# Optimization experiments

Hardware: AMD Instinct MI355X
Metric: run time of the kernel (lower is better)

The kernel has to match this reference:

```python
import jax, jax.numpy as jnp
import numpy as np

B, S, D = 2, 2048, 1024
H = 16
HD = D // H

def setup_inputs() -> dict:
    key = jax.random.key(0)
    k1, k2, k3 = jax.random.split(key, 3)
    x = jax.random.normal(k1, (B, S, D), dtype=jnp.float32)
    w_attn = jax.random.normal(k2, (D, 3 * D), dtype=jnp.float32) * (1.0 / np.sqrt(D))
    b_attn = jnp.zeros((3 * D,), dtype=jnp.float32)
    w_proj = jax.random.normal(k3, (D, D), dtype=jnp.float32) * (1.0 / np.sqrt(D))
    b_proj = jnp.zeros((D,), dtype=jnp.float32)
    return {"x": x, "w_attn": w_attn, "b_attn": b_attn, "w_proj": w_proj, "b_proj": b_proj}

def reference(x, w_attn, b_attn, w_proj, b_proj):
    bsz, seq_len, embed_dim = x.shape
    qkv = x @ w_attn + b_attn                      # [B,S,3D]
    q, k, v = jnp.split(qkv, 3, axis=-1)
    # [B,S,D] -> [B,H,S,HD]
    def heads(t):
        return t.reshape(bsz, seq_len, H, HD).transpose(0, 2, 1, 3)
    q, k, v = heads(q), heads(k), heads(v)
    scale = 1.0 / np.sqrt(HD)
    att = jnp.einsum('bhqd,bhkd->bhqk', q, k) * scale  # [B,H,S,S]
    causal = jnp.tril(jnp.ones((seq_len, seq_len), dtype=bool))
    att = jnp.where(causal[None, None], att, jnp.float32(-jnp.inf))
    att = jax.nn.softmax(att, axis=-1)
    y = jnp.einsum('bhqk,bhkd->bhqd', att, v)          # [B,H,S,HD]
    y = y.transpose(0, 2, 1, 3).reshape(bsz, seq_len, embed_dim)
    return y @ w_proj + b_proj
```

## Files before the change

kernel.cpp:

```cpp
#include <hip/hip_runtime.h>
#include <hip/hip_bf16.h>
#include <math.h>

typedef __bf16 bf16x8 __attribute__((ext_vector_type(8)));
typedef float f32x4 __attribute__((ext_vector_type(4)));

#define LOG2E 1.44269504088896340736f

#define SEQ 2048
#define DMODEL 1024
#define NH 16
#define HD 64

__device__ __forceinline__ void gl2lds16(const void* g, void* l) {
  __builtin_amdgcn_global_load_lds((__attribute__((address_space(1))) void*)g,
                                   (__attribute__((address_space(3))) void*)l,
                                   16, 0, 0);
}

__global__ void detect_dtype(const unsigned* __restrict__ x, unsigned* __restrict__ flag) {
  __shared__ int cnt[256];
  int c = 0;
  for (int i = threadIdx.x; i < 4096; i += 256) {
    unsigned e = (x[i] >> 23) & 0xFF;
    c += (e >= 0x70 && e <= 0x8F) ? 1 : 0;
  }
  cnt[threadIdx.x] = c;
  __syncthreads();
  for (int s = 128; s > 0; s >>= 1) {
    if ((int)threadIdx.x < s) cnt[threadIdx.x] += cnt[threadIdx.x + s];
    __syncthreads();
  }
  if (threadIdx.x == 0) flag[0] = (cnt[0] > 2048) ? 1u : 0u;
}

__global__ void conv_to_bf16(const void* __restrict__ in, __hip_bfloat16* __restrict__ out,
                             int n, const unsigned* __restrict__ flag) {
  const int i = (blockIdx.x * 256 + threadIdx.x) * 4;
  if (i >= n) return;
  if (*flag) {
    const float4 v = *(const float4*)((const float*)in + i);
    out[i + 0] = __float2bfloat16(v.x);
    out[i + 1] = __float2bfloat16(v.y);
    out[i + 2] = __float2bfloat16(v.z);
    out[i + 3] = __float2bfloat16(v.w);
  } else {
    const __hip_bfloat16* bin = (const __hip_bfloat16*)in;
    out[i + 0] = bin[i + 0];
    out[i + 1] = bin[i + 1];
    out[i + 2] = bin[i + 2];
    out[i + 3] = bin[i + 3];
  }
}

__global__ void transpose_cvt(const void* __restrict__ in, __hip_bfloat16* __restrict__ out,
                              int R, int C, const unsigned* __restrict__ flag) {
  __shared__ __hip_bfloat16 tile[64][65];
  const bool f32 = (*flag != 0);
  const int c0 = blockIdx.x * 64, r0 = blockIdx.y * 64;
  const int tx = threadIdx.x & 63, ty = threadIdx.x >> 6;
#pragma unroll
  for (int i = 0; i < 16; ++i) {
    int r = ty + i * 4;
    long idx = (long)(r0 + r) * C + c0 + tx;
    tile[r][tx] = f32 ? __float2bfloat16(((const float*)in)[idx])
                      : ((const __hip_bfloat16*)in)[idx];
  }
  __syncthreads();
#pragma unroll
  for (int i = 0; i < 16; ++i) {
    int r = ty + i * 4;
    out[(long)(c0 + r) * R + r0 + tx] = tile[tx][r];
  }
}

template <int MODE>
__global__ __launch_bounds__(256, 2) void gemm_bt(
    const __hip_bfloat16* __restrict__ A, const __hip_bfloat16* __restrict__ Bt,
    const __hip_bfloat16* __restrict__ bias, void* __restrict__ C,
    __hip_bfloat16* __restrict__ q_ws, __hip_bfloat16* __restrict__ k_ws,
    __hip_bfloat16* __restrict__ vt_ws, int M, int N, int K,
    const unsigned* __restrict__ flag) {
  alignas(16) __shared__ __hip_bfloat16 lA[128 * 32];
  alignas(16) __shared__ __hip_bfloat16 lB[128 * 32];
  const int tid = threadIdx.x;
  const int wave = tid >> 6, lane = tid & 63;
  const int l15 = lane & 15, lq = lane >> 4;
  const int m0 = blockIdx.y * 128, n0 = blockIdx.x * 128;
  const int wrow = (wave >> 1) * 64, wcol = (wave & 1) * 64;

  const __hip_bfloat16* ap0 = A + (long)(m0 + wave * 16 + (lane >> 2)) * K + (lane & 3) * 8;
  const __hip_bfloat16* bp0 = Bt + (long)(n0 + wave * 16 + (lane >> 2)) * K + (lane & 3) * 8;
  __hip_bfloat16* lA0 = lA + wave * 512;
  __hip_bfloat16* lA1 = lA + (wave + 4) * 512;
  __hip_bfloat16* lB0 = lB + wave * 512;
  __hip_bfloat16* lB1 = lB + (wave + 4) * 512;

  f32x4 acc[4][4];
#pragma unroll
  for (int i = 0; i < 4; ++i)
#pragma unroll
    for (int j = 0; j < 4; ++j) acc[i][j] = {0.f, 0.f, 0.f, 0.f};

  for (int k0 = 0; k0 < K; k0 += 32) {
    __syncthreads();
    gl2lds16(ap0 + k0, lA0);
    gl2lds16(ap0 + (long)64 * K + k0, lA1);
    gl2lds16(bp0 + k0, lB0);
    gl2lds16(bp0 + (long)64 * K + k0, lB1);
    __syncthreads();
    bf16x8 af[4], bfr[4];
#pragma unroll
    for (int i = 0; i < 4; ++i)
      af[i] = *(const bf16x8*)(lA + (wrow + 16 * i + l15) * 32 + lq * 8);
#pragma unroll
    for (int j = 0; j < 4; ++j)
      bfr[j] = *(const bf16x8*)(lB + (wcol + 16 * j + l15) * 32 + lq * 8);
#pragma unroll
    for (int i = 0; i < 4; ++i)
#pragma unroll
      for (int j = 0; j < 4; ++j)
        acc[i][j] = __builtin_amdgcn_mfma_f32_16x16x32_bf16(af[i], bfr[j], acc[i][j], 0, 0, 0);
  }

  const bool outf32 = (MODE == 0) && (*flag != 0);
#pragma unroll
  for (int i = 0; i < 4; ++i) {
    const int row = m0 + wrow + 16 * i + lq * 4;
#pragma unroll
    for (int j = 0; j < 4; ++j) {
      const int col = n0 + wcol + 16 * j + l15;
      const float bv = __bfloat162float(bias[col]);
#pragma unroll
      for (int r = 0; r < 4; ++r) {
        const float v = acc[i][j][r] + bv;
        const int rr = row + r;
        if (MODE == 0) {
          if (outf32)
            ((float*)C)[(long)rr * N + col] = v;
          else
            ((__hip_bfloat16*)C)[(long)rr * N + col] = __float2bfloat16(v);
        } else {
          const int which = col >> 10;
          const int f = col & 1023;
          const int h = f >> 6, d = f & 63;
          const int b = rr >> 11, s = rr & 2047;
          const long bh = (long)b * NH + h;
          const __hip_bfloat16 hv = __float2bfloat16(v);
          if (which == 0)
            q_ws[(bh * SEQ + s) * HD + d] = hv;
          else if (which == 1)
            k_ws[(bh * SEQ + s) * HD + d] = hv;
          else
            vt_ws[(bh * HD + d) * SEQ + s] = hv;
        }
      }
    }
  }
}

__global__ __launch_bounds__(256, 4) void attn_fused(
    const __hip_bfloat16* __restrict__ q_ws, const __hip_bfloat16* __restrict__ k_ws,
    const __hip_bfloat16* __restrict__ vt_ws, __hip_bfloat16* __restrict__ y_ws) {
  alignas(16) __shared__ __hip_bfloat16 lK[2][64 * 64];
  alignas(16) __shared__ __hip_bfloat16 lV[2][64 * 64];
  alignas(16) __shared__ __hip_bfloat16 lP[4][16 * 72];
  const int tid = threadIdx.x, wave = tid >> 6, lane = tid & 63;
  const int l15 = lane & 15, lq = lane >> 4;
  const int bh = blockIdx.x >> 4, pair = blockIdx.x & 15;
  const __hip_bfloat16* Qb = q_ws + (long)bh * SEQ * HD;
  const __hip_bfloat16* Kb = k_ws + (long)bh * SEQ * HD;
  const __hip_bfloat16* Vb = vt_ws + (long)bh * HD * SEQ;
  __hip_bfloat16* lPw = lP[wave];
  const int b = bh >> 4, h = bh & 15;
  const float SCL = 0.125f * LOG2E;

  const int p0 = wave * 16 + (lane >> 3);
  const int cl = lane & 7;

#pragma unroll 1
  for (int phase = 0; phase < 2; ++phase) {
    const int qt = phase ? (31 - pair) : pair;
    const int q0 = qt * 64;
    const int nkt = qt + 1;

    const int qrow = q0 + wave * 16 + l15;
    const bf16x8 qa0 = *(const bf16x8*)(Qb + (long)qrow * HD + lq * 8);
    const bf16x8 qa1 = *(const bf16x8*)(Qb + (long)qrow * HD + 32 + lq * 8);

    f32x4 accO[4];
#pragma unroll
    for (int j = 0; j < 4; ++j) accO[j] = {0.f, 0.f, 0.f, 0.f};
    float l_part[4];
#pragma unroll
    for (int r = 0; r < 4; ++r) l_part[r] = 0.f;

#pragma unroll
    for (int i = 0; i < 2; ++i) {
      const int p = p0 + i * 8;
      const int c = cl ^ (p & 7);
      gl2lds16(Kb + (long)p * HD + c * 8, &lK[0][(wave * 16 + i * 8) * 64]);
      gl2lds16(Vb + (long)p * SEQ + c * 8, &lV[0][(wave * 16 + i * 8) * 64]);
    }
    __syncthreads();

#pragma unroll 1
    for (int kt = 0; kt < nkt; ++kt) {
      const int buf = kt & 1;
      if (kt + 1 < nkt) {
        const int kb = (kt + 1) * 64;
#pragma unroll
        for (int i = 0; i < 2; ++i) {
          const int p = p0 + i * 8;
          const int c = cl ^ (p & 7);
          gl2lds16(Kb + (long)(kb + p) * HD + c * 8, &lK[buf ^ 1][(wave * 16 + i * 8) * 64]);
          gl2lds16(Vb + (long)p * SEQ + kb + c * 8, &lV[buf ^ 1][(wave * 16 + i * 8) * 64]);
        }
      }
      const __hip_bfloat16* lKb = lK[buf];
      const __hip_bfloat16* lVb = lV[buf];

      f32x4 sf[4];
#pragma unroll
      for (int jt = 0; jt < 4; ++jt) {
        sf[jt] = {0.f, 0.f, 0.f, 0.f};
        const int pp = jt * 16 + l15;
        const bf16x8 kb0 = *(const bf16x8*)(lKb + (pp * 8 + (lq ^ (pp & 7))) * 8);
        const bf16x8 kb1 = *(const bf16x8*)(lKb + (pp * 8 + ((4 + lq) ^ (pp & 7))) * 8);
        sf[jt] = __builtin_amdgcn_mfma_f32_16x16x32_bf16(qa0, kb0, sf[jt], 0, 0, 0);
        sf[jt] = __builtin_amdgcn_mfma_f32_16x16x32_bf16(qa1, kb1, sf[jt], 0, 0, 0);
      }

      const bool diag = (kt == nkt - 1);
#pragma unroll
      for (int r = 0; r < 4; ++r) {
        float p[4];
#pragma unroll
        for (int jt = 0; jt < 4; ++jt) p[jt] = exp2f(sf[jt][r] * SCL);
        if (diag) {
          const int rloc = wave * 16 + lq * 4 + r;
#pragma unroll
          for (int jt = 0; jt < 4; ++jt) {
            const int col = jt * 16 + l15;
            p[jt] = (col <= rloc) ? p[jt] : 0.f;
          }
        }
        l_part[r] += (p[0] + p[1]) + (p[2] + p[3]);
#pragma unroll
        for (int jt = 0; jt < 4; ++jt)
          lPw[(lq * 4 + r) * 72 + jt * 16 + l15] = __float2bfloat16(p[jt]);
      }

      const bf16x8 pa0 = *(const bf16x8*)(lPw + l15 * 72 + lq * 8);
      const bf16x8 pa1 = *(const bf16x8*)(lPw + l15 * 72 + 32 + lq * 8);
#pragma unroll
      for (int j = 0; j < 4; ++j) {
        const int d = j * 16 + l15;
        const bf16x8 vb0 = *(const bf16x8*)(lVb + (d * 8 + (lq ^ (d & 7))) * 8);
        const bf16x8 vb1 = *(const bf16x8*)(lVb + (d * 8 + ((4 + lq) ^ (d & 7))) * 8);
        accO[j] = __builtin_amdgcn_mfma_f32_16x16x32_bf16(pa0, vb0, accO[j], 0, 0, 0);
        accO[j] = __builtin_amdgcn_mfma_f32_16x16x32_bf16(pa1, vb1, accO[j], 0, 0, 0);
      }
      __syncthreads();
    }

#pragma unroll
    for (int r = 0; r < 4; ++r) {
      float l = l_part[r];
#pragma unroll
      for (int off = 1; off < 16; off <<= 1) l += __shfl_xor(l, off, 64);
      const float inv = 1.f / l;
      const int s = q0 + wave * 16 + lq * 4 + r;
#pragma unroll
      for (int j = 0; j < 4; ++j) {
        const float v = accO[j][r] * inv;
        y_ws[((long)(b * SEQ + s)) * DMODEL + h * HD + j * 16 + l15] = __float2bfloat16(v);
      }
    }
  }
}

extern "C" void kernel_launch(void* const* d_in, const int* in_sizes, int n_in,
                              void* d_out, int out_size, void* d_ws, size_t ws_size,
                              hipStream_t stream) {
  const void* x = d_in[0];
  const void* w_attn = d_in[1];
  const void* b_attn = d_in[2];
  const void* w_proj = d_in[3];
  const void* b_proj = d_in[4];

  char* ws = (char*)d_ws;
  const size_t MB = 1024 * 1024;
  unsigned* flag = (unsigned*)ws;
  __hip_bfloat16* wT_attn = (__hip_bfloat16*)(ws + 1 * MB);
  __hip_bfloat16* wT_proj = (__hip_bfloat16*)(ws + 7 * MB);
  __hip_bfloat16* x_bf = (__hip_bfloat16*)(ws + 9 * MB);
  __hip_bfloat16* q_ws = (__hip_bfloat16*)(ws + 17 * MB);
  __hip_bfloat16* k_ws = (__hip_bfloat16*)(ws + 25 * MB);
  __hip_bfloat16* vt_ws = (__hip_bfloat16*)(ws + 33 * MB);
  __hip_bfloat16* y_ws = (__hip_bfloat16*)(ws + 41 * MB);
  __hip_bfloat16* bA_bf = (__hip_bfloat16*)(ws + 49 * MB);
  __hip_bfloat16* bP_bf = (__hip_bfloat16*)(ws + 49 * MB + 8192);

  detect_dtype<<<1, 256, 0, stream>>>((const unsigned*)x, flag);

  conv_to_bf16<<<4096, 256, 0, stream>>>(x, x_bf, 4194304, flag);
  conv_to_bf16<<<3, 256, 0, stream>>>(b_attn, bA_bf, 3072, flag);
  conv_to_bf16<<<1, 256, 0, stream>>>(b_proj, bP_bf, 1024, flag);
  transpose_cvt<<<dim3(3072 / 64, 1024 / 64), 256, 0, stream>>>(w_attn, wT_attn, 1024, 3072, flag);
  transpose_cvt<<<dim3(1024 / 64, 1024 / 64), 256, 0, stream>>>(w_proj, wT_proj, 1024, 1024, flag);

  gemm_bt<1><<<dim3(3072 / 128, 4096 / 128), 256, 0, stream>>>(
      x_bf, wT_attn, bA_bf, nullptr, q_ws, k_ws, vt_ws, 4096, 3072, 1024, flag);

  attn_fused<<<dim3(512), 256, 0, stream>>>(q_ws, k_ws, vt_ws, y_ws);

  gemm_bt<0><<<dim3(1024 / 128, 4096 / 128), 256, 0, stream>>>(
      y_ws, wT_proj, bP_bf, d_out, nullptr, nullptr, nullptr, 4096, 1024, 1024, flag);
}
```

Measured before the change: 227.6 us.

## Compute transposed scores to keep P in registers and permute V layout

The attention kernel now computes S^T (K as the A operand, Q as B), so each lane's softmax outputs line up with the B-operand layout of the PV MFMA. That removes the per-wave LDS round trip for P. The QKV GEMM writes V^T with a permuted sequence order within each 32-element group, so the register-resident P columns match the V fragments. The grid also changes from 512 blocks that each process a paired short and long query tile to 1024 blocks that each handle one tile, with heavy tiles scheduled first. Output stores become 4-wide vectors and the row-sum reduction needs fewer shuffles.

```diff
diff --git a/kernel.cpp b/kernel.cpp
--- a/kernel.cpp
+++ b/kernel.cpp
@@ -3,6 +3,7 @@
 #include <math.h>
 
 typedef __bf16 bf16x8 __attribute__((ext_vector_type(8)));
+typedef __bf16 bf16x4 __attribute__((ext_vector_type(4)));
 typedef float f32x4 __attribute__((ext_vector_type(4)));
 
 #define LOG2E 1.44269504088896340736f
@@ -151,8 +152,14 @@
             q_ws[(bh * SEQ + s) * HD + d] = hv;
           else if (which == 1)
             k_ws[(bh * SEQ + s) * HD + d] = hv;
-          else
-            vt_ws[(bh * HD + d) * SEQ + s] = hv;
+          else {
+            const int w = s & 31;
+            const int wl = w & 15;
+            const int sig = (w >> 4) ? (2 * (wl & ~3) + 4 + (wl & 3))
+                                     : (2 * (wl & ~3) + (wl & 3));
+            const int sp = (s & ~31) | sig;
+            vt_ws[(bh * HD + d) * SEQ + sp] = hv;
+          }
         }
       }
     }
@@ -164,119 +171,110 @@
     const __hip_bfloat16* __restrict__ vt_ws, __hip_bfloat16* __restrict__ y_ws) {
   alignas(16) __shared__ __hip_bfloat16 lK[2][64 * 64];
   alignas(16) __shared__ __hip_bfloat16 lV[2][64 * 64];
-  alignas(16) __shared__ __hip_bfloat16 lP[4][16 * 72];
   const int tid = threadIdx.x, wave = tid >> 6, lane = tid & 63;
   const int l15 = lane & 15, lq = lane >> 4;
-  const int bh = blockIdx.x >> 4, pair = blockIdx.x & 15;
+  const int qt = 31 - (blockIdx.x >> 5);
+  const int bh = blockIdx.x & 31;
+  const int q0 = qt * 64;
+  const int nkt = qt + 1;
   const __hip_bfloat16* Qb = q_ws + (long)bh * SEQ * HD;
   const __hip_bfloat16* Kb = k_ws + (long)bh * SEQ * HD;
   const __hip_bfloat16* Vb = vt_ws + (long)bh * HD * SEQ;
-  __hip_bfloat16* lPw = lP[wave];
   const int b = bh >> 4, h = bh & 15;
   const float SCL = 0.125f * LOG2E;
 
+  const int qrow = q0 + wave * 16 + l15;
+  const bf16x8 qa0 = *(const bf16x8*)(Qb + (long)qrow * HD + lq * 8);
+  const bf16x8 qa1 = *(const bf16x8*)(Qb + (long)qrow * HD + 32 + lq * 8);
+
+  f32x4 accO[4];
+#pragma unroll
+  for (int j = 0; j < 4; ++j) accO[j] = {0.f, 0.f, 0.f, 0.f};
+  float l_part = 0.f;
+
   const int p0 = wave * 16 + (lane >> 3);
   const int cl = lane & 7;
 
+#pragma unroll
+  for (int i = 0; i < 2; ++i) {
+    const int p = p0 + i * 8;
+    const int c = cl ^ (p & 7);
+    gl2lds16(Kb + (long)p * HD + c * 8, &lK[0][(wave * 16 + i * 8) * 64]);
+    gl2lds16(Vb + (long)p * SEQ + c * 8, &lV[0][(wave * 16 + i * 8) * 64]);
+  }
+  __syncthreads();
+
 #pragma unroll 1
-  for (int phase = 0; phase < 2; ++phase) {
-    const int qt = phase ? (31 - pair) : pair;
-    const int q0 = qt * 64;
-    const int nkt = qt + 1;
-
-    const int qrow = q0 + wave * 16 + l15;
-    const bf16x8 qa0 = *(const bf16x8*)(Qb + (long)qrow * HD + lq * 8);
-    const bf16x8 qa1 = *(const bf16x8*)(Qb + (long)qrow * HD + 32 + lq * 8);
-
-    f32x4 accO[4];
-#pragma unroll
-    for (int j = 0; j < 4; ++j) accO[j] = {0.f, 0.f, 0.f, 0.f};
-    float l_part[4];
-#pragma unroll
-    for (int r = 0; r < 4; ++r) l_part[r] = 0.f;
-
-#pragma unroll
-    for (int i = 0; i < 2; ++i) {
-      const int p = p0 + i * 8;
-      const int c = cl ^ (p & 7);
-      gl2lds16(Kb + (long)p * HD + c * 8, &lK[0][(wave * 16 + i * 8) * 64]);
-      gl2lds16(Vb + (long)p * SEQ + c * 8, &lV[0][(wave * 16 + i * 8) * 64]);
-    }
-    __syncthreads();
-
-#pragma unroll 1
-    for (int kt = 0; kt < nkt; ++kt) {
-      const int buf = kt & 1;
-      if (kt + 1 < nkt) {
-        const int kb = (kt + 1) * 64;
-#pragma unroll
-        for (int i = 0; i < 2; ++i) {
-          const int p = p0 + i * 8;
-          const int c = cl ^ (p & 7);
-          gl2lds16(Kb + (long)(kb + p) * HD + c * 8, &lK[buf ^ 1][(wave * 16 + i * 8) * 64]);
-          gl2lds16(Vb + (long)p * SEQ + kb + c * 8, &lV[buf ^ 1][(wave * 16 + i * 8) * 64]);
+  for (int kt = 0; kt < nkt; ++kt) {
+    const int buf = kt & 1;
+    if (kt + 1 < nkt) {
+      const int kb = (kt + 1) * 64;
+#pragma unroll
+      for (int i = 0; i < 2; ++i) {
+        const int p = p0 + i * 8;
+        const int c = cl ^ (p & 7);
+        gl2lds16(Kb + (long)(kb + p) * HD + c * 8, &lK[buf ^ 1][(wave * 16 + i * 8) * 64]);
+        gl2lds16(Vb + (long)p * SEQ + kb + c * 8, &lV[buf ^ 1][(wave * 16 + i * 8) * 64]);
+      }
+    }
+    const __hip_bfloat16* lKb = lK[buf];
+    const __hip_bfloat16* lVb = lV[buf];
+
+    f32x4 st[4];
+#pragma unroll
+    for (int t = 0; t < 4; ++t) {
+      st[t] = {0.f, 0.f, 0.f, 0.f};
+      const int pp = t * 16 + l15;
+      const bf16x8 kb0 = *(const bf16x8*)(lKb + (pp * 8 + (lq ^ (pp & 7))) * 8);
+      const bf16x8 kb1 = *(const bf16x8*)(lKb + (pp * 8 + ((4 + lq) ^ (pp & 7))) * 8);
+      st[t] = __builtin_amdgcn_mfma_f32_16x16x32_bf16(kb0, qa0, st[t], 0, 0, 0);
+      st[t] = __builtin_amdgcn_mfma_f32_16x16x32_bf16(kb1, qa1, st[t], 0, 0, 0);
+    }
+
+    const bool diag = (kt == nkt - 1);
+    const int qloc = wave * 16 + l15;
+    bf16x8 pb[2];
+#pragma unroll
+    for (int c = 0; c < 2; ++c) {
+#pragma unroll
+      for (int t2 = 0; t2 < 2; ++t2) {
+        const int tt = c * 2 + t2;
+#pragma unroll
+        for (int r = 0; r < 4; ++r) {
+          float pv = exp2f(st[tt][r] * SCL);
+          if (diag) {
+            const int colloc = tt * 16 + lq * 4 + r;
+            pv = (colloc <= qloc) ? pv : 0.f;
+          }
+          l_part += pv;
+          pb[c][t2 * 4 + r] = (__bf16)pv;
         }
       }
-      const __hip_bfloat16* lKb = lK[buf];
-      const __hip_bfloat16* lVb = lV[buf];
-
-      f32x4 sf[4];
-#pragma unroll
-      for (int jt = 0; jt < 4; ++jt) {
-        sf[jt] = {0.f, 0.f, 0.f, 0.f};
-        const int pp = jt * 16 + l15;
-        const bf16x8 kb0 = *(const bf16x8*)(lKb + (pp * 8 + (lq ^ (pp & 7))) * 8);
-        const bf16x8 kb1 = *(const bf16x8*)(lKb + (pp * 8 + ((4 + lq) ^ (pp & 7))) * 8);
-        sf[jt] = __builtin_amdgcn_mfma_f32_16x16x32_bf16(qa0, kb0, sf[jt], 0, 0, 0);
-        sf[jt] = __builtin_amdgcn_mfma_f32_16x16x32_bf16(qa1, kb1, sf[jt], 0, 0, 0);
-      }
-
-      const bool diag = (kt == nkt - 1);
-#pragma unroll
-      for (int r = 0; r < 4; ++r) {
-        float p[4];
-#pragma unroll
-        for (int jt = 0; jt < 4; ++jt) p[jt] = exp2f(sf[jt][r] * SCL);
-        if (diag) {
-          const int rloc = wave * 16 + lq * 4 + r;
-#pragma unroll
-          for (int jt = 0; jt < 4; ++jt) {
-            const int col = jt * 16 + l15;
-            p[jt] = (col <= rloc) ? p[jt] : 0.f;
-          }
-        }
-        l_part[r] += (p[0] + p[1]) + (p[2] + p[3]);
-#pragma unroll
-        for (int jt = 0; jt < 4; ++jt)
-          lPw[(lq * 4 + r) * 72 + jt * 16 + l15] = __float2bfloat16(p[jt]);
-      }
-
-      const bf16x8 pa0 = *(const bf16x8*)(lPw + l15 * 72 + lq * 8);
-      const bf16x8 pa1 = *(const bf16x8*)(lPw + l15 * 72 + 32 + lq * 8);
-#pragma unroll
-      for (int j = 0; j < 4; ++j) {
-        const int d = j * 16 + l15;
-        const bf16x8 vb0 = *(const bf16x8*)(lVb + (d * 8 + (lq ^ (d & 7))) * 8);
-        const bf16x8 vb1 = *(const bf16x8*)(lVb + (d * 8 + ((4 + lq) ^ (d & 7))) * 8);
-        accO[j] = __builtin_amdgcn_mfma_f32_16x16x32_bf16(pa0, vb0, accO[j], 0, 0, 0);
-        accO[j] = __builtin_amdgcn_mfma_f32_16x16x32_bf16(pa1, vb1, accO[j], 0, 0, 0);
-      }
-      __syncthreads();
-    }
-
-#pragma unroll
-    for (int r = 0; r < 4; ++r) {
-      float l = l_part[r];
-#pragma unroll
-      for (int off = 1; off < 16; off <<= 1) l += __shfl_xor(l, off, 64);
-      const float inv = 1.f / l;
-      const int s = q0 + wave * 16 + lq * 4 + r;
-#pragma unroll
-      for (int j = 0; j < 4; ++j) {
-        const float v = accO[j][r] * inv;
-        y_ws[((long)(b * SEQ + s)) * DMODEL + h * HD + j * 16 + l15] = __float2bfloat16(v);
-      }
-    }
+    }
+
+#pragma unroll
+    for (int j = 0; j < 4; ++j) {
+      const int d = j * 16 + l15;
+      const bf16x8 va0 = *(const bf16x8*)(lVb + (d * 8 + (lq ^ (d & 7))) * 8);
+      const bf16x8 va1 = *(const bf16x8*)(lVb + (d * 8 + ((4 + lq) ^ (d & 7))) * 8);
+      accO[j] = __builtin_amdgcn_mfma_f32_16x16x32_bf16(va0, pb[0], accO[j], 0, 0, 0);
+      accO[j] = __builtin_amdgcn_mfma_f32_16x16x32_bf16(va1, pb[1], accO[j], 0, 0, 0);
+    }
+    __syncthreads();
+  }
+
+  float l = l_part;
+  l += __shfl_xor(l, 16, 64);
+  l += __shfl_xor(l, 32, 64);
+  const float inv = 1.f / l;
+  const int s = q0 + wave * 16 + l15;
+  __hip_bfloat16* yb = y_ws + (long)(b * SEQ + s) * DMODEL + h * HD;
+#pragma unroll
+  for (int j = 0; j < 4; ++j) {
+    bf16x4 o;
+#pragma unroll
+    for (int r = 0; r < 4; ++r) o[r] = (__bf16)(accO[j][r] * inv);
+    *(bf16x4*)(yb + j * 16 + lq * 4) = o;
   }
 }
 
@@ -313,7 +311,7 @@
   gemm_bt<1><<<dim3(3072 / 128, 4096 / 128), 256, 0, stream>>>(
       x_bf, wT_attn, bA_bf, nullptr, q_ws, k_ws, vt_ws, 4096, 3072, 1024, flag);
 
-  attn_fused<<<dim3(512), 256, 0, stream>>>(q_ws, k_ws, vt_ws, y_ws);
+  attn_fused<<<dim3(1024), 256, 0, stream>>>(q_ws, k_ws, vt_ws, y_ws);
 
   gemm_bt<0><<<dim3(1024 / 128, 4096 / 128), 256, 0, stream>>>(
       y_ws, wT_proj, bP_bf, d_out, nullptr, nullptr, nullptr, 4096, 1024, 1024, flag);
```

New measurement: 213.1 us. -6.4%, faster.
